# Optimization experiments

Measured on AMD Instinct MI355X. Metric: run time of the kernel, lower is better.

## Reference

```python
import jax, jax.numpy as jnp
import numpy as np

N = 20000      # nodes
E = 640000     # edges
FIN = 256
FQK = 256


def setup_inputs() -> dict:
    key = jax.random.key(0)
    kx, ks, kd, kw = jax.random.split(key, 4)
    x = jax.random.normal(kx, (N, FIN), dtype=jnp.float32)
    # src must be sorted (original scatter_softmax assumes grouped index);
    # force last element to N-1 so nbatches == N as in batch[-1]+1.
    src = jnp.sort(jax.random.randint(ks, (E,), 0, N))
    src = src.at[-1].set(N - 1)
    dest = jax.random.randint(kd, (E,), 0, N)
    ei = jnp.stack([src, dest]).astype(jnp.int64)
    # nn.Linear(Fin, 2*Fqk, bias=False) weight: [2*Fqk, Fin]
    bound = 1.0 / np.sqrt(FIN)
    W = jax.random.uniform(kw, (2 * FQK, FIN), dtype=jnp.float32,
                           minval=-bound, maxval=bound)
    return {"x": x, "ei": ei, "W": W}


def reference(x, ei, W):
    src, dest = ei[0], ei[1]
    n_nodes = x.shape[0]
    scaling = FQK ** -0.5
    qk = x @ W.T                      # [N, 2*Fqk]
    q, k = jnp.split(qk, 2, axis=-1)  # each [N, Fqk]
    q = q * scaling
    # per-edge dot product: (q[src] . k[dest])  -> [E]
    aw = jnp.einsum('ef,ef->e', q[src], k[dest])
    # scatter softmax over edges grouped by src node (raw exp, as original)
    ex = jnp.exp(aw)
    expsum = jax.ops.segment_sum(ex, src, num_segments=n_nodes)  # [N]
    return ex / expsum[src]
```

## Files before the change

### kernel.cpp

```cpp
#include <hip/hip_runtime.h>
#include <cmath>

#define FIN 256
#define FQK 256
#define SCALING 0.0625f
#define MAX_SEG 256

typedef __bf16 bf16_t;
typedef bf16_t bf16x8 __attribute__((ext_vector_type(8)));
typedef float  f32x4  __attribute__((ext_vector_type(4)));

__device__ __forceinline__ unsigned short f2bf(float f) {
    unsigned int u = __float_as_uint(f);
    u += 0x7FFFu + ((u >> 16) & 1u);
    return (unsigned short)(u >> 16);
}
__device__ __forceinline__ float bf_lo(unsigned int w) { return __uint_as_float(w << 16); }
__device__ __forceinline__ float bf_hi(unsigned int w) { return __uint_as_float(w & 0xFFFF0000u); }

__global__ __launch_bounds__(FIN) void compute_M_kernel(const float* __restrict__ W,
                                                        unsigned short* __restrict__ Mb) {
    const int f = blockIdx.x;
    const int g = threadIdx.x;
    const float* __restrict__ Wq = W;
    const float* __restrict__ Wk = W + FQK * FIN;
    float acc = 0.f;
#pragma unroll 8
    for (int c = 0; c < FQK; ++c) {
        acc += Wq[c * FIN + f] * Wk[c * FIN + g];
    }
    Mb[f * FIN + g] = f2bf(acc * SCALING);
}

#define ASTRIDE 40

__global__ __launch_bounds__(256) void gemm_y_kernel(const float* __restrict__ x,
                                                     const unsigned short* __restrict__ Mb,
                                                     unsigned short* __restrict__ y, int N) {
    __shared__ unsigned short sA[64 * ASTRIDE];

    const int t    = threadIdx.x;
    const int wv   = t >> 6;
    const int lane = t & 63;
    const int q    = lane >> 4;
    const int m16  = lane & 15;
    const int n0   = blockIdx.x * 64;
    const int f0   = wv * 64;

    f32x4 acc[4][4] = {};

    const int srow = t >> 2;
    const int skc  = (t & 3) * 8;

    for (int kc = 0; kc < FIN; kc += 32) {
        {
            const int n = n0 + srow;
            float4 v0 = make_float4(0.f, 0.f, 0.f, 0.f), v1 = v0;
            if (n < N) {
                v0 = *(const float4*)(x + (size_t)n * FIN + kc + skc);
                v1 = *(const float4*)(x + (size_t)n * FIN + kc + skc + 4);
            }
            unsigned short* p = &sA[srow * ASTRIDE + skc];
            p[0] = f2bf(v0.x); p[1] = f2bf(v0.y); p[2] = f2bf(v0.z); p[3] = f2bf(v0.w);
            p[4] = f2bf(v1.x); p[5] = f2bf(v1.y); p[6] = f2bf(v1.z); p[7] = f2bf(v1.w);
        }
        __syncthreads();

        bf16x8 afrag[4];
#pragma unroll
        for (int mt = 0; mt < 4; ++mt) {
            const int row = mt * 16 + m16;
            afrag[mt] = *(const bf16x8*)&sA[row * ASTRIDE + q * 8];
        }
#pragma unroll
        for (int ft = 0; ft < 4; ++ft) {
            const int f = f0 + ft * 16 + m16;
            union { uint4 u; bf16x8 v; } bu;
            bu.u = *(const uint4*)(Mb + (size_t)f * FIN + kc + q * 8);
#pragma unroll
            for (int mt = 0; mt < 4; ++mt)
                acc[mt][ft] = __builtin_amdgcn_mfma_f32_16x16x32_bf16(afrag[mt], bu.v,
                                                                     acc[mt][ft], 0, 0, 0);
        }
        __syncthreads();
    }

#pragma unroll
    for (int mt = 0; mt < 4; ++mt) {
#pragma unroll
        for (int r = 0; r < 4; ++r) {
            const int n = n0 + mt * 16 + q * 4 + r;
            if (n < N) {
#pragma unroll
                for (int ft = 0; ft < 4; ++ft)
                    y[(size_t)n * FIN + f0 + ft * 16 + m16] = f2bf(acc[mt][ft][r]);
            }
        }
    }
}

__global__ __launch_bounds__(256) void seg_kernel(const int* __restrict__ src,
                                                  int* __restrict__ seg, int N, int E) {
    const int n = blockIdx.x * 256 + threadIdx.x;
    if (n > N) return;
    int lo = 0, hi = E;
    while (lo < hi) {
        const int mid = (lo + hi) >> 1;
        if (src[mid] < n) lo = mid + 1; else hi = mid;
    }
    seg[n] = lo;
}

__global__ __launch_bounds__(256) void node_edge_kernel(const float* __restrict__ x,
                                                        const unsigned short* __restrict__ y,
                                                        const int* __restrict__ dest,
                                                        const int* __restrict__ seg,
                                                        float* __restrict__ out, int N) {
    __shared__ float exlds[4][MAX_SEG];

    const int w    = threadIdx.x >> 6;
    const int lane = threadIdx.x & 63;
    const int n    = blockIdx.x * 4 + w;
    const int g    = lane >> 4;
    const int j    = lane & 15;

    int   s0 = 0, cnt = 0;
    float inv = 0.f;

    if (n < N) {
        s0 = seg[n];
        cnt = seg[n + 1] - s0;
    }

    if (cnt > 0) {
        float4 xf[4];
#pragma unroll
        for (int u = 0; u < 2; ++u) {
            xf[u * 2 + 0] = *(const float4*)(x + (size_t)n * FIN + u * 128 + j * 8);
            xf[u * 2 + 1] = *(const float4*)(x + (size_t)n * FIN + u * 128 + j * 8 + 4);
        }

        float sum = 0.f;
        for (int base = 0; base < cnt; base += 64) {
            const int m = min(64, cnt - base);
            const int vd = (lane < m) ? dest[s0 + base + lane] : 0;
            const int nit = (m + 3) >> 2;
            for (int it = 0; it < nit; ++it) {
                const int  eg    = it * 4 + g;
                const bool valid = eg < m;
                const int  d     = __shfl(vd, eg, 64);
                const uint4* __restrict__ yr = (const uint4*)(y + (size_t)(valid ? d : 0) * FIN);
                float acc = 0.f;
#pragma unroll
                for (int u = 0; u < 2; ++u) {
                    const uint4 qv = yr[u * 16 + j];
                    const float4 xa = xf[u * 2 + 0];
                    const float4 xb = xf[u * 2 + 1];
                    acc += bf_lo(qv.x) * xa.x + bf_hi(qv.x) * xa.y
                         + bf_lo(qv.y) * xa.z + bf_hi(qv.y) * xa.w
                         + bf_lo(qv.z) * xb.x + bf_hi(qv.z) * xb.y
                         + bf_lo(qv.w) * xb.z + bf_hi(qv.w) * xb.w;
                }
                acc += __shfl_xor(acc, 1, 64);
                acc += __shfl_xor(acc, 2, 64);
                acc += __shfl_xor(acc, 4, 64);
                acc += __shfl_xor(acc, 8, 64);
                if (valid) {
                    const float ex = __expf(acc);
                    sum += ex;
                    const int idx = base + eg;
                    if (j == 0 && idx < MAX_SEG) exlds[w][idx] = ex;
                }
            }
        }
        sum += __shfl_xor(sum, 16, 64);
        sum += __shfl_xor(sum, 32, 64);
        inv = 1.0f / sum;
    }

    __syncthreads();

    if (cnt > 0) {
        const int lim = cnt < MAX_SEG ? cnt : MAX_SEG;
        for (int i = lane; i < lim; i += 64)
            out[s0 + i] = exlds[w][i] * inv;
    }
}

extern "C" void kernel_launch(void* const* d_in, const int* in_sizes, int n_in,
                              void* d_out, int out_size, void* d_ws, size_t ws_size,
                              hipStream_t stream) {
    const float* x  = (const float*)d_in[0];
    const int*   ei = (const int*)d_in[1];
    const float* W  = (const float*)d_in[2];
    float* out = (float*)d_out;

    const int N = in_sizes[0] / FIN;
    const int E = in_sizes[1] / 2;

    unsigned short* Mb = (unsigned short*)d_ws;
    unsigned short* y  = Mb + (size_t)FIN * FIN;
    int*            seg = (int*)(y + (size_t)N * FIN);

    compute_M_kernel<<<FIN, FIN, 0, stream>>>(W, Mb);

    gemm_y_kernel<<<(N + 63) / 64, 256, 0, stream>>>(x, Mb, y, N);

    seg_kernel<<<(N + 256) / 256, 256, 0, stream>>>(ei, seg, N, E);

    node_edge_kernel<<<(N + 3) / 4, 256, 0, stream>>>(x, y, ei + E, seg, out, N);
}
```

Baseline: 138.6 us.

## Fuse segment search into edge kernel, widen per-edge gather, shrink GEMM tile

Removes the separate seg_kernel launch by having two lanes of each wavefront binary-search the src boundaries inside the node-edge kernel. The edge loop now processes 8 edges per iteration with 8 lanes per edge, each lane loading four 16-byte chunks of the y row, which is meant to raise memory-level parallelism on the gathers. The GEMM tile drops from 64 to 32 rows per block, doubling the block count for better occupancy at the cost of less reuse of the M matrix. It also adds redundant binary-search work per node and higher register use from holding 8 float4 of x per lane.

```diff
diff --git a/kernel.cpp b/kernel.cpp
--- a/kernel.cpp
+++ b/kernel.cpp
@@ -33,52 +33,47 @@
 }
 
 #define ASTRIDE 40
+#define GROWS   32
 
 __global__ __launch_bounds__(256) void gemm_y_kernel(const float* __restrict__ x,
                                                      const unsigned short* __restrict__ Mb,
                                                      unsigned short* __restrict__ y, int N) {
-    __shared__ unsigned short sA[64 * ASTRIDE];
+    __shared__ unsigned short sA[GROWS * ASTRIDE];
 
     const int t    = threadIdx.x;
     const int wv   = t >> 6;
     const int lane = t & 63;
     const int q    = lane >> 4;
     const int m16  = lane & 15;
-    const int n0   = blockIdx.x * 64;
+    const int n0   = blockIdx.x * GROWS;
     const int f0   = wv * 64;
 
-    f32x4 acc[4][4] = {};
-
-    const int srow = t >> 2;
-    const int skc  = (t & 3) * 8;
+    f32x4 acc[2][4] = {};
+
+    const int srow = t >> 3;
+    const int skc  = (t & 7) * 4;
 
     for (int kc = 0; kc < FIN; kc += 32) {
         {
             const int n = n0 + srow;
-            float4 v0 = make_float4(0.f, 0.f, 0.f, 0.f), v1 = v0;
-            if (n < N) {
-                v0 = *(const float4*)(x + (size_t)n * FIN + kc + skc);
-                v1 = *(const float4*)(x + (size_t)n * FIN + kc + skc + 4);
-            }
+            float4 v = make_float4(0.f, 0.f, 0.f, 0.f);
+            if (n < N) v = *(const float4*)(x + (size_t)n * FIN + kc + skc);
             unsigned short* p = &sA[srow * ASTRIDE + skc];
-            p[0] = f2bf(v0.x); p[1] = f2bf(v0.y); p[2] = f2bf(v0.z); p[3] = f2bf(v0.w);
-            p[4] = f2bf(v1.x); p[5] = f2bf(v1.y); p[6] = f2bf(v1.z); p[7] = f2bf(v1.w);
+            p[0] = f2bf(v.x); p[1] = f2bf(v.y); p[2] = f2bf(v.z); p[3] = f2bf(v.w);
         }
         __syncthreads();
 
-        bf16x8 afrag[4];
-#pragma unroll
-        for (int mt = 0; mt < 4; ++mt) {
-            const int row = mt * 16 + m16;
-            afrag[mt] = *(const bf16x8*)&sA[row * ASTRIDE + q * 8];
-        }
+        bf16x8 afrag[2];
+#pragma unroll
+        for (int mt = 0; mt < 2; ++mt)
+            afrag[mt] = *(const bf16x8*)&sA[(mt * 16 + m16) * ASTRIDE + q * 8];
 #pragma unroll
         for (int ft = 0; ft < 4; ++ft) {
             const int f = f0 + ft * 16 + m16;
             union { uint4 u; bf16x8 v; } bu;
             bu.u = *(const uint4*)(Mb + (size_t)f * FIN + kc + q * 8);
 #pragma unroll
-            for (int mt = 0; mt < 4; ++mt)
+            for (int mt = 0; mt < 2; ++mt)
                 acc[mt][ft] = __builtin_amdgcn_mfma_f32_16x16x32_bf16(afrag[mt], bu.v,
                                                                      acc[mt][ft], 0, 0, 0);
         }
@@ -86,7 +81,7 @@
     }
 
 #pragma unroll
-    for (int mt = 0; mt < 4; ++mt) {
+    for (int mt = 0; mt < 2; ++mt) {
 #pragma unroll
         for (int r = 0; r < 4; ++r) {
             const int n = n0 + mt * 16 + q * 4 + r;
@@ -99,72 +94,71 @@
     }
 }
 
-__global__ __launch_bounds__(256) void seg_kernel(const int* __restrict__ src,
-                                                  int* __restrict__ seg, int N, int E) {
-    const int n = blockIdx.x * 256 + threadIdx.x;
-    if (n > N) return;
-    int lo = 0, hi = E;
-    while (lo < hi) {
-        const int mid = (lo + hi) >> 1;
-        if (src[mid] < n) lo = mid + 1; else hi = mid;
-    }
-    seg[n] = lo;
-}
-
 __global__ __launch_bounds__(256) void node_edge_kernel(const float* __restrict__ x,
                                                         const unsigned short* __restrict__ y,
+                                                        const int* __restrict__ src,
                                                         const int* __restrict__ dest,
-                                                        const int* __restrict__ seg,
-                                                        float* __restrict__ out, int N) {
+                                                        float* __restrict__ out,
+                                                        int N, int E) {
     __shared__ float exlds[4][MAX_SEG];
 
     const int w    = threadIdx.x >> 6;
     const int lane = threadIdx.x & 63;
     const int n    = blockIdx.x * 4 + w;
-    const int g    = lane >> 4;
-    const int j    = lane & 15;
-
-    int   s0 = 0, cnt = 0;
+    const int s    = lane >> 3;
+    const int j    = lane & 7;
+
+    int bound = 0;
+    if (lane < 2) {
+        const int target = n + lane;
+        int lo = 0, hi = E;
+        while (lo < hi) {
+            const int mid = (lo + hi) >> 1;
+            if (src[mid] < target) lo = mid + 1; else hi = mid;
+        }
+        bound = lo;
+    }
+    const int s0 = __shfl(bound, 0, 64);
+    const int s1 = __shfl(bound, 1, 64);
+    const int cnt = (n < N) ? (s1 - s0) : 0;
+
     float inv = 0.f;
 
-    if (n < N) {
-        s0 = seg[n];
-        cnt = seg[n + 1] - s0;
-    }
-
     if (cnt > 0) {
-        float4 xf[4];
-#pragma unroll
-        for (int u = 0; u < 2; ++u) {
-            xf[u * 2 + 0] = *(const float4*)(x + (size_t)n * FIN + u * 128 + j * 8);
-            xf[u * 2 + 1] = *(const float4*)(x + (size_t)n * FIN + u * 128 + j * 8 + 4);
+        float4 xf[8];
+#pragma unroll
+        for (int i = 0; i < 4; ++i) {
+            const int off = (i * 8 + j) * 8;
+            xf[i * 2 + 0] = *(const float4*)(x + (size_t)n * FIN + off);
+            xf[i * 2 + 1] = *(const float4*)(x + (size_t)n * FIN + off + 4);
         }
 
         float sum = 0.f;
         for (int base = 0; base < cnt; base += 64) {
             const int m = min(64, cnt - base);
             const int vd = (lane < m) ? dest[s0 + base + lane] : 0;
-            const int nit = (m + 3) >> 2;
+            const int nit = (m + 7) >> 3;
             for (int it = 0; it < nit; ++it) {
-                const int  eg    = it * 4 + g;
+                const int  eg    = it * 8 + s;
                 const bool valid = eg < m;
                 const int  d     = __shfl(vd, eg, 64);
                 const uint4* __restrict__ yr = (const uint4*)(y + (size_t)(valid ? d : 0) * FIN);
+                uint4 qv[4];
+#pragma unroll
+                for (int i = 0; i < 4; ++i) qv[i] = yr[i * 8 + j];
                 float acc = 0.f;
 #pragma unroll
-                for (int u = 0; u < 2; ++u) {
-                    const uint4 qv = yr[u * 16 + j];
-                    const float4 xa = xf[u * 2 + 0];
-                    const float4 xb = xf[u * 2 + 1];
-                    acc += bf_lo(qv.x) * xa.x + bf_hi(qv.x) * xa.y
-                         + bf_lo(qv.y) * xa.z + bf_hi(qv.y) * xa.w
-                         + bf_lo(qv.z) * xb.x + bf_hi(qv.z) * xb.y
-                         + bf_lo(qv.w) * xb.z + bf_hi(qv.w) * xb.w;
+                for (int i = 0; i < 4; ++i) {
+                    const float4 xa = xf[i * 2 + 0];
+                    const float4 xb = xf[i * 2 + 1];
+                    acc += bf_lo(qv[i].x) * xa.x + bf_hi(qv[i].x) * xa.y
+                         + bf_lo(qv[i].y) * xa.z + bf_hi(qv[i].y) * xa.w
+                         + bf_lo(qv[i].z) * xb.x + bf_hi(qv[i].z) * xb.y
+                         + bf_lo(qv[i].w) * xb.z + bf_hi(qv[i].w) * xb.w;
                 }
                 acc += __shfl_xor(acc, 1, 64);
                 acc += __shfl_xor(acc, 2, 64);
                 acc += __shfl_xor(acc, 4, 64);
-                acc += __shfl_xor(acc, 8, 64);
                 if (valid) {
                     const float ex = __expf(acc);
                     sum += ex;
@@ -173,6 +167,7 @@
                 }
             }
         }
+        sum += __shfl_xor(sum, 8, 64);
         sum += __shfl_xor(sum, 16, 64);
         sum += __shfl_xor(sum, 32, 64);
         inv = 1.0f / sum;
@@ -200,13 +195,10 @@
 
     unsigned short* Mb = (unsigned short*)d_ws;
     unsigned short* y  = Mb + (size_t)FIN * FIN;
-    int*            seg = (int*)(y + (size_t)N * FIN);
 
     compute_M_kernel<<<FIN, FIN, 0, stream>>>(W, Mb);
 
-    gemm_y_kernel<<<(N + 63) / 64, 256, 0, stream>>>(x, Mb, y, N);
-
-    seg_kernel<<<(N + 256) / 256, 256, 0, stream>>>(ei, seg, N, E);
-
-    node_edge_kernel<<<(N + 3) / 4, 256, 0, stream>>>(x, y, ei + E, seg, out, N);
-}
+    gemm_y_kernel<<<(N + GROWS - 1) / GROWS, 256, 0, stream>>>(x, Mb, y, N);
+
+    node_edge_kernel<<<(N + 3) / 4, 256, 0, stream>>>(x, y, ei, ei + E, out, N, E);
+}
```

After: 152.4 us. 10.0% more time.
